# Performance work log

Measured on AMD Instinct MI355X. Metric: run time of the kernel, lower is better.

The kernel has to match this reference:

```python
import jax, jax.numpy as jnp
import numpy as np

N_NODES = 50000
N_EDGES = 800000
IN_CH, HID_CH, OUT_CH = 128, 128, 64


def setup_inputs() -> dict:
    key = jax.random.key(0)
    ks = jax.random.split(key, 8)
    x = jax.random.normal(ks[0], (N_NODES, IN_CH), dtype=jnp.float32)
    edge_index = jax.random.randint(ks[1], (2, N_EDGES), 0, N_NODES, dtype=jnp.int64)
    # PyG SAGEConv params: lin_l (applied to aggregated neighbors, has bias),
    # lin_r (applied to root node, no bias). Stored here as [in, out] matrices.
    s1 = 1.0 / np.sqrt(IN_CH)
    s2 = 1.0 / np.sqrt(HID_CH)
    W1l = jax.random.uniform(ks[2], (IN_CH, HID_CH), jnp.float32, -s1, s1)
    b1 = jnp.zeros((HID_CH,), jnp.float32)
    W1r = jax.random.uniform(ks[3], (IN_CH, HID_CH), jnp.float32, -s1, s1)
    W2l = jax.random.uniform(ks[4], (HID_CH, OUT_CH), jnp.float32, -s2, s2)
    b2 = jnp.zeros((OUT_CH,), jnp.float32)
    W2r = jax.random.uniform(ks[5], (HID_CH, OUT_CH), jnp.float32, -s2, s2)
    return {"x": x, "edge_index": edge_index, "W1l": W1l, "b1": b1,
            "W1r": W1r, "W2l": W2l, "b2": b2, "W2r": W2r}


def _sage_conv(x, src, dst, Wl, b, Wr):
    # mean-aggregate source features onto targets, then linear transform
    msg = x[src]                                        # [E, d] gather
    agg = jax.ops.segment_sum(msg, dst, num_segments=N_NODES)   # [N, d]
    deg = jax.ops.segment_sum(jnp.ones((src.shape[0],), x.dtype), dst,
                              num_segments=N_NODES)     # [N]
    mean = agg / jnp.maximum(deg, 1.0)[:, None]
    return mean @ Wl + b + x @ Wr


def reference(x, edge_index, W1l, b1, W1r, W2l, b2, W2r):
    src, dst = edge_index[0], edge_index[1]
    h = jax.nn.relu(_sage_conv(x, src, dst, W1l, b1, W1r))
    # F.dropout(p=0.3) is identity in eval mode
    return _sage_conv(h, src, dst, W2l, b2, W2r)
```

## Files before the change

kernel.cpp:

```cpp
#include <hip/hip_runtime.h>
#include <hip/hip_bf16.h>


#define TBLOCK 256
#define MAXBUCK 1024
#define BUILD_GRID 512

typedef __attribute__((ext_vector_type(8))) short short8;
typedef __attribute__((ext_vector_type(4))) float f32x4;

__device__ __forceinline__ float bf2f(ushort u) {
    union { unsigned int i; float f; } v;
    v.i = (unsigned int)u << 16;
    return v.f;
}
__device__ __forceinline__ ushort f2bf(float f) {
    union { float f; unsigned int u; } v;
    v.f = f;
    unsigned int r = v.u + 0x7fffu + ((v.u >> 16) & 1u);
    return (ushort)(r >> 16);
}

__device__ __forceinline__ int block_detect_is64(const int* __restrict__ edges) {
    __shared__ int sbad[4];
    __shared__ int sflag;
    int tid = threadIdx.x;
    int bad = 0;
    for (int i = tid; i < 2048; i += TBLOCK)
        if (edges[2 * i + 1] != 0) bad = 1;
    unsigned long long b = __ballot(bad);
    if ((tid & 63) == 0) sbad[tid >> 6] = (b != 0) ? 1 : 0;
    __syncthreads();
    if (tid == 0) sflag = (sbad[0] | sbad[1] | sbad[2] | sbad[3]) ? 0 : 1;
    __syncthreads();
    return sflag;
}

__device__ __forceinline__ int load_src(const int* e, long long i, int E, int is64) {
    return is64 ? e[2 * i] : e[i];
}
__device__ __forceinline__ int load_dst(const int* e, long long i, int E, int is64) {
    return is64 ? e[2 * (long long)E + 2 * i] : e[(long long)E + i];
}

__global__ __launch_bounds__(TBLOCK) void histA_k(const int* __restrict__ edges, int E,
                                                  int* __restrict__ hist, int NBUCK) {
    int is64 = block_detect_is64(edges);
    __shared__ int lh[MAXBUCK];
    int t = threadIdx.x;
    for (int i = t; i < NBUCK; i += TBLOCK) lh[i] = 0;
    __syncthreads();
    int per = (E + gridDim.x - 1) / gridDim.x;
    int b0 = blockIdx.x * per, b1 = min(E, b0 + per);
    for (int i = b0 + t; i < b1; i += TBLOCK) {
        int d = load_dst(edges, i, E, is64);
        atomicAdd(&lh[d >> 8], 1);
    }
    __syncthreads();
    for (int i = t; i < NBUCK; i += TBLOCK)
        if (lh[i]) atomicAdd(&hist[i], lh[i]);
}

__global__ __launch_bounds__(TBLOCK) void scanB_k(const int* __restrict__ hist,
                                                  int* __restrict__ base,
                                                  int* __restrict__ cursor, int NBUCK) {
    __shared__ int s[TBLOCK];
    int t = threadIdx.x;
    int v[4];
    int sum = 0;
#pragma unroll
    for (int i = 0; i < 4; i++) {
        int idx = t * 4 + i;
        int d = (idx < NBUCK) ? hist[idx] : 0;
        v[i] = sum;
        sum += d;
    }
    s[t] = sum;
    __syncthreads();
    for (int off = 1; off < TBLOCK; off <<= 1) {
        int x = (t >= off) ? s[t - off] : 0;
        __syncthreads();
        s[t] += x;
        __syncthreads();
    }
    int excl = (t == 0) ? 0 : s[t - 1];
#pragma unroll
    for (int i = 0; i < 4; i++) {
        int idx = t * 4 + i;
        if (idx < NBUCK) {
            int b = excl + v[i];
            base[idx] = b;
            cursor[idx] = b;
        }
    }
    if (t == TBLOCK - 1) base[NBUCK] = s[TBLOCK - 1];
}

__global__ __launch_bounds__(TBLOCK) void scatterA_k(const int* __restrict__ edges, int E,
                                                     int* __restrict__ cursor,
                                                     unsigned int* __restrict__ packed,
                                                     int NBUCK) {
    int is64 = block_detect_is64(edges);
    __shared__ int lh[MAXBUCK];
    __shared__ int lb[MAXBUCK];
    int t = threadIdx.x;
    for (int i = t; i < NBUCK; i += TBLOCK) lh[i] = 0;
    __syncthreads();
    int per = (E + gridDim.x - 1) / gridDim.x;
    int b0 = blockIdx.x * per, b1 = min(E, b0 + per);
    for (int i = b0 + t; i < b1; i += TBLOCK) {
        int d = load_dst(edges, i, E, is64);
        atomicAdd(&lh[d >> 8], 1);
    }
    __syncthreads();
    for (int i = t; i < NBUCK; i += TBLOCK) {
        int c = lh[i];
        lb[i] = c ? atomicAdd(&cursor[i], c) : 0;
        lh[i] = 0;
    }
    __syncthreads();
    for (int i = b0 + t; i < b1; i += TBLOCK) {
        int s = load_src(edges, i, E, is64);
        int d = load_dst(edges, i, E, is64);
        int b = d >> 8;
        int pos = lb[b] + atomicAdd(&lh[b], 1);
        packed[pos] = (unsigned int)s | ((unsigned int)(d & 255) << 24);
    }
}

__global__ __launch_bounds__(TBLOCK) void buildB_k(const unsigned int* __restrict__ packed,
                                                   const int* __restrict__ base,
                                                   int* __restrict__ offs,
                                                   int* __restrict__ degi,
                                                   float* __restrict__ invdeg,
                                                   int* __restrict__ csr, int N) {
    __shared__ int cnt[TBLOCK], scn[TBLOCK], cur[TBLOCK];
    int t = threadIdx.x;
    int bucket = blockIdx.x;
    int e0 = base[bucket], e1 = base[bucket + 1];
    cnt[t] = 0;
    cur[t] = 0;
    __syncthreads();
    for (int i = e0 + t; i < e1; i += TBLOCK)
        atomicAdd(&cnt[packed[i] >> 24], 1);
    __syncthreads();
    scn[t] = cnt[t];
    __syncthreads();
    for (int off = 1; off < TBLOCK; off <<= 1) {
        int x = (t >= off) ? scn[t - off] : 0;
        __syncthreads();
        scn[t] += x;
        __syncthreads();
    }
    int excl = (t == 0) ? 0 : scn[t - 1];
    int node = bucket * 256 + t;
    if (node < N) {
        offs[node] = e0 + excl;
        degi[node] = cnt[t];
        invdeg[node] = 1.0f / fmaxf((float)cnt[t], 1.0f);
    }
    __syncthreads();
    cnt[t] = excl;
    __syncthreads();
    for (int i = e0 + t; i < e1; i += TBLOCK) {
        unsigned int p = packed[i];
        int nl = p >> 24;
        int pos = e0 + cnt[nl] + atomicAdd(&cur[nl], 1);
        csr[pos] = (int)(p & 0xFFFFFFu);
    }
}

__global__ __launch_bounds__(TBLOCK) void prep_k(const float* __restrict__ x,
                                                 const float* __restrict__ W1l,
                                                 const float* __restrict__ W1r,
                                                 const float* __restrict__ W2l,
                                                 const float* __restrict__ W2r,
                                                 ushort* __restrict__ xb,
                                                 ushort* __restrict__ wc1,
                                                 ushort* __restrict__ wc2,
                                                 int n8, int nxb) {
    if ((int)blockIdx.x < nxb) {
        int i = blockIdx.x * TBLOCK + threadIdx.x;
        if (i >= n8) return;
        const float4* p = (const float4*)x + (size_t)i * 2;
        float4 a = p[0], b = p[1];
        short8 o;
        o[0] = f2bf(a.x); o[1] = f2bf(a.y); o[2] = f2bf(a.z); o[3] = f2bf(a.w);
        o[4] = f2bf(b.x); o[5] = f2bf(b.y); o[6] = f2bf(b.z); o[7] = f2bf(b.w);
        *(short8*)(xb + (size_t)i * 8) = o;
    } else {
        int i = (blockIdx.x - nxb) * TBLOCK + threadIdx.x;
        if (i < 32768) {
            int j = i & 7;
            int rest = i >> 3;
            int n = rest & 127;
            int k = ((rest >> 7) << 3) | j;
            float w = (k < 128) ? W1l[k * 128 + n] : W1r[(k - 128) * 128 + n];
            wc1[i] = f2bf(w);
        } else if (i < 49152) {
            int i2 = i - 32768;
            int j = i2 & 7;
            int rest = i2 >> 3;
            int n = rest & 127;
            int k = ((rest >> 7) << 3) | j;
            float w = (n < 64) ? W2l[k * 64 + n] : W2r[k * 64 + (n - 64)];
            wc2[i2] = f2bf(w);
        }
    }
}

template <int C, bool ACCUM>
__global__ __launch_bounds__(TBLOCK) void gatherb_k(const ushort* __restrict__ feat,
                                                    const int* __restrict__ csr,
                                                    const int* __restrict__ offs,
                                                    const int* __restrict__ degi,
                                                    const float* __restrict__ invdeg,
                                                    ushort* __restrict__ outB,
                                                    float* __restrict__ outF, int N) {
    constexpr int G = C / 8;
    constexpr int NPB = TBLOCK / G;
    int n = blockIdx.x * NPB + threadIdx.x / G;
    if (n >= N) return;
    int lane = threadIdx.x % G;
    int c = lane * 8;
    int s0 = offs[n];
    int d = degi[n];
    float acc[8] = {0.f, 0.f, 0.f, 0.f, 0.f, 0.f, 0.f, 0.f};
    for (int base = 0; base < d; base += G) {
        int rem = d - base;
        int my = (lane < rem) ? csr[s0 + base + lane] : 0;
        if (rem >= G) {
#pragma unroll
            for (int j = 0; j < G; j++) {
                int s = __shfl(my, j, G);
                short8 v = *(const short8*)(feat + (size_t)s * C + c);
#pragma unroll
                for (int q = 0; q < 8; q++) acc[q] += bf2f((ushort)v[q]);
            }
        } else {
            for (int j = 0; j < rem; j++) {
                int s = __shfl(my, j, G);
                short8 v = *(const short8*)(feat + (size_t)s * C + c);
#pragma unroll
                for (int q = 0; q < 8; q++) acc[q] += bf2f((ushort)v[q]);
            }
        }
    }
    float sc = invdeg[n];
    if (ACCUM) {
        float* o = outF + (size_t)n * C + c;
        float4 p0 = *(float4*)o;
        float4 p1 = *(float4*)(o + 4);
        p0.x += sc * acc[0]; p0.y += sc * acc[1]; p0.z += sc * acc[2]; p0.w += sc * acc[3];
        p1.x += sc * acc[4]; p1.y += sc * acc[5]; p1.z += sc * acc[6]; p1.w += sc * acc[7];
        *(float4*)o = p0;
        *(float4*)(o + 4) = p1;
    } else {
        short8 o;
#pragma unroll
        for (int q = 0; q < 8; q++) o[q] = f2bf(sc * acc[q]);
        *(short8*)(outB + (size_t)n * C + c) = o;
    }
}

template <int KTOT, int EPI>
__global__ __launch_bounds__(TBLOCK) void gemm_k(const ushort* __restrict__ A0,
                                                 const ushort* __restrict__ A1,
                                                 const ushort* __restrict__ wc,
                                                 const float* __restrict__ bias,
                                                 ushort* __restrict__ outB,
                                                 float* __restrict__ outF, int N) {
    __shared__ __align__(16) ushort sW[KTOT * 128];
    for (int i = threadIdx.x * 8; i < KTOT * 128; i += TBLOCK * 8)
        *(short8*)&sW[i] = *(const short8*)&wc[i];
    __syncthreads();

    const int wave = threadIdx.x >> 6;
    const int lane = threadIdx.x & 63;
    const int quad = lane >> 4;
    const int l16 = lane & 15;
    const int m0 = (blockIdx.x * 4 + wave) * 32;
    if (m0 >= N) return;

    f32x4 acc[2][8];
#pragma unroll
    for (int t = 0; t < 2; t++)
#pragma unroll
        for (int nt = 0; nt < 8; nt++) acc[t][nt] = (f32x4){0.f, 0.f, 0.f, 0.f};

    const int k0q = quad * 8;
#pragma unroll
    for (int kb = 0; kb < KTOT; kb += 32) {
        int k = kb + k0q;
        const ushort* abase = (KTOT == 256 && k >= 128) ? (A1 + (k - 128)) : (A0 + k);
        short8 a[2];
#pragma unroll
        for (int t = 0; t < 2; t++) {
            int m = m0 + t * 16 + l16;
            if (m > N - 1) m = N - 1;
            a[t] = *(const short8*)(abase + (size_t)m * 128);
        }
#pragma unroll
        for (int nt = 0; nt < 8; nt++) {
            short8 b = *(const short8*)&sW[((k >> 3) * 128 + nt * 16 + l16) * 8];
            acc[0][nt] = __builtin_amdgcn_mfma_f32_16x16x32_bf16(a[0], b, acc[0][nt], 0, 0, 0);
            acc[1][nt] = __builtin_amdgcn_mfma_f32_16x16x32_bf16(a[1], b, acc[1][nt], 0, 0, 0);
        }
    }

#pragma unroll
    for (int t = 0; t < 2; t++) {
#pragma unroll
        for (int r = 0; r < 4; r++) {
            int m = m0 + t * 16 + quad * 4 + r;
            if (m >= N) continue;
#pragma unroll
            for (int nt = 0; nt < 8; nt++) {
                int n = nt * 16 + l16;
                float v = acc[t][nt][r];
                if (EPI == 1) {
                    v = fmaxf(v + bias[n], 0.f);
                    outB[(size_t)m * 128 + n] = f2bf(v);
                } else {
                    if (n < 64) outB[(size_t)m * 64 + n] = f2bf(v);
                    else outF[(size_t)m * 64 + (n - 64)] = v + bias[n - 64];
                }
            }
        }
    }
}

extern "C" void kernel_launch(void* const* d_in, const int* in_sizes, int n_in,
                              void* d_out, int out_size, void* d_ws, size_t ws_size,
                              hipStream_t stream) {
    const float* x = (const float*)d_in[0];
    const int* edges = (const int*)d_in[1];
    const float* W1l = (const float*)d_in[2];
    const float* b1 = (const float*)d_in[3];
    const float* W1r = (const float*)d_in[4];
    const float* W2l = (const float*)d_in[5];
    const float* b2 = (const float*)d_in[6];
    const float* W2r = (const float*)d_in[7];
    float* out = (float*)d_out;

    const int N = in_sizes[0] / 128;
    const int E = in_sizes[1] / 2;
    const int Na = (N + 63) & ~63;
    const int NBUCK = (N + 255) >> 8;

    char* W = (char*)d_ws;
    size_t off = 0;
    auto alloc = [&](size_t bytes) {
        void* p = W + off;
        off = (off + bytes + 255) & ~(size_t)255;
        return p;
    };
    int* hist = (int*)alloc((size_t)MAXBUCK * 4);
    size_t zbytes = off;
    int* base = (int*)alloc((size_t)(MAXBUCK + 1) * 4);
    int* cursor = (int*)alloc((size_t)MAXBUCK * 4);
    int* offs = (int*)alloc((size_t)Na * 4);
    int* degi = (int*)alloc((size_t)Na * 4);
    float* invdeg = (float*)alloc((size_t)Na * 4);
    unsigned int* packed = (unsigned int*)alloc((size_t)E * 4);
    int* csr = (int*)alloc((size_t)E * 4);
    ushort* xb = (ushort*)alloc((size_t)N * 128 * 2);
    ushort* agg1b = (ushort*)alloc((size_t)N * 128 * 2);
    ushort* hb = (ushort*)alloc((size_t)N * 128 * 2);
    ushort* t2b = (ushort*)alloc((size_t)N * 64 * 2);
    ushort* wc1 = (ushort*)alloc(32768 * 2);
    ushort* wc2 = (ushort*)alloc(16384 * 2);

    hipMemsetAsync(d_ws, 0, zbytes, stream);

    histA_k<<<BUILD_GRID, TBLOCK, 0, stream>>>(edges, E, hist, NBUCK);
    scanB_k<<<1, TBLOCK, 0, stream>>>(hist, base, cursor, NBUCK);
    scatterA_k<<<BUILD_GRID, TBLOCK, 0, stream>>>(edges, E, cursor, packed, NBUCK);
    buildB_k<<<NBUCK, TBLOCK, 0, stream>>>(packed, base, offs, degi, invdeg, csr, N);

    const int n8 = N * 128 / 8;
    const int nxb = (n8 + TBLOCK - 1) / TBLOCK;
    prep_k<<<nxb + 192, TBLOCK, 0, stream>>>(x, W1l, W1r, W2l, W2r, xb, wc1, wc2, n8, nxb);

    gatherb_k<128, false><<<(N + 15) / 16, TBLOCK, 0, stream>>>(
        xb, csr, offs, degi, invdeg, agg1b, nullptr, N);
    gemm_k<256, 1><<<(N + 127) / 128, TBLOCK, 0, stream>>>(
        agg1b, xb, wc1, b1, hb, nullptr, N);

    gemm_k<128, 2><<<(N + 127) / 128, TBLOCK, 0, stream>>>(
        hb, nullptr, wc2, b2, t2b, out, N);
    gatherb_k<64, true><<<(N + 31) / 32, TBLOCK, 0, stream>>>(
        t2b, csr, offs, degi, invdeg, nullptr, out, N);
}
```

Before: 215.9 us.

## Fuse CSR build and bf16 prep into one cooperative kernel with grid syncs

```diff
diff --git a/kernel.cpp b/kernel.cpp
--- a/kernel.cpp
+++ b/kernel.cpp
@@ -1,5 +1,8 @@
 #include <hip/hip_runtime.h>
 #include <hip/hip_bf16.h>
+#include <hip/hip_cooperative_groups.h>
+
+namespace cg = cooperative_groups;
 
 
 #define TBLOCK 256
@@ -21,21 +24,6 @@
     return (ushort)(r >> 16);
 }
 
-__device__ __forceinline__ int block_detect_is64(const int* __restrict__ edges) {
-    __shared__ int sbad[4];
-    __shared__ int sflag;
-    int tid = threadIdx.x;
-    int bad = 0;
-    for (int i = tid; i < 2048; i += TBLOCK)
-        if (edges[2 * i + 1] != 0) bad = 1;
-    unsigned long long b = __ballot(bad);
-    if ((tid & 63) == 0) sbad[tid >> 6] = (b != 0) ? 1 : 0;
-    __syncthreads();
-    if (tid == 0) sflag = (sbad[0] | sbad[1] | sbad[2] | sbad[3]) ? 0 : 1;
-    __syncthreads();
-    return sflag;
-}
-
 __device__ __forceinline__ int load_src(const int* e, long long i, int E, int is64) {
     return is64 ? e[2 * i] : e[i];
 }
@@ -43,153 +31,42 @@
     return is64 ? e[2 * (long long)E + 2 * i] : e[(long long)E + i];
 }
 
-__global__ __launch_bounds__(TBLOCK) void histA_k(const int* __restrict__ edges, int E,
-                                                  int* __restrict__ hist, int NBUCK) {
-    int is64 = block_detect_is64(edges);
-    __shared__ int lh[MAXBUCK];
-    int t = threadIdx.x;
-    for (int i = t; i < NBUCK; i += TBLOCK) lh[i] = 0;
-    __syncthreads();
-    int per = (E + gridDim.x - 1) / gridDim.x;
-    int b0 = blockIdx.x * per, b1 = min(E, b0 + per);
-    for (int i = b0 + t; i < b1; i += TBLOCK) {
-        int d = load_dst(edges, i, E, is64);
-        atomicAdd(&lh[d >> 8], 1);
-    }
-    __syncthreads();
-    for (int i = t; i < NBUCK; i += TBLOCK)
-        if (lh[i]) atomicAdd(&hist[i], lh[i]);
-}
-
-__global__ __launch_bounds__(TBLOCK) void scanB_k(const int* __restrict__ hist,
-                                                  int* __restrict__ base,
-                                                  int* __restrict__ cursor, int NBUCK) {
-    __shared__ int s[TBLOCK];
-    int t = threadIdx.x;
-    int v[4];
-    int sum = 0;
-#pragma unroll
-    for (int i = 0; i < 4; i++) {
-        int idx = t * 4 + i;
-        int d = (idx < NBUCK) ? hist[idx] : 0;
-        v[i] = sum;
-        sum += d;
-    }
-    s[t] = sum;
-    __syncthreads();
-    for (int off = 1; off < TBLOCK; off <<= 1) {
-        int x = (t >= off) ? s[t - off] : 0;
-        __syncthreads();
-        s[t] += x;
-        __syncthreads();
-    }
-    int excl = (t == 0) ? 0 : s[t - 1];
-#pragma unroll
-    for (int i = 0; i < 4; i++) {
-        int idx = t * 4 + i;
-        if (idx < NBUCK) {
-            int b = excl + v[i];
-            base[idx] = b;
-            cursor[idx] = b;
-        }
-    }
-    if (t == TBLOCK - 1) base[NBUCK] = s[TBLOCK - 1];
-}
-
-__global__ __launch_bounds__(TBLOCK) void scatterA_k(const int* __restrict__ edges, int E,
-                                                     int* __restrict__ cursor,
-                                                     unsigned int* __restrict__ packed,
-                                                     int NBUCK) {
-    int is64 = block_detect_is64(edges);
+__global__ __launch_bounds__(TBLOCK) void build_k(
+    const float* __restrict__ x,
+    const float* __restrict__ W1l, const float* __restrict__ W1r,
+    const float* __restrict__ W2l, const float* __restrict__ W2r,
+    const int* __restrict__ edges, int E, int N, int NBUCK,
+    ushort* __restrict__ xb, ushort* __restrict__ wc1, ushort* __restrict__ wc2,
+    int* __restrict__ hist, int* __restrict__ baseg, int* __restrict__ cursor,
+    unsigned int* __restrict__ packed,
+    int* __restrict__ offs, int* __restrict__ degi, float* __restrict__ invdeg,
+    int* __restrict__ csr, int n8) {
+    cg::grid_group grid = cg::this_grid();
     __shared__ int lh[MAXBUCK];
     __shared__ int lb[MAXBUCK];
-    int t = threadIdx.x;
-    for (int i = t; i < NBUCK; i += TBLOCK) lh[i] = 0;
-    __syncthreads();
-    int per = (E + gridDim.x - 1) / gridDim.x;
-    int b0 = blockIdx.x * per, b1 = min(E, b0 + per);
-    for (int i = b0 + t; i < b1; i += TBLOCK) {
-        int d = load_dst(edges, i, E, is64);
-        atomicAdd(&lh[d >> 8], 1);
-    }
-    __syncthreads();
-    for (int i = t; i < NBUCK; i += TBLOCK) {
-        int c = lh[i];
-        lb[i] = c ? atomicAdd(&cursor[i], c) : 0;
-        lh[i] = 0;
-    }
-    __syncthreads();
-    for (int i = b0 + t; i < b1; i += TBLOCK) {
-        int s = load_src(edges, i, E, is64);
-        int d = load_dst(edges, i, E, is64);
-        int b = d >> 8;
-        int pos = lb[b] + atomicAdd(&lh[b], 1);
-        packed[pos] = (unsigned int)s | ((unsigned int)(d & 255) << 24);
-    }
-}
-
-__global__ __launch_bounds__(TBLOCK) void buildB_k(const unsigned int* __restrict__ packed,
-                                                   const int* __restrict__ base,
-                                                   int* __restrict__ offs,
-                                                   int* __restrict__ degi,
-                                                   float* __restrict__ invdeg,
-                                                   int* __restrict__ csr, int N) {
-    __shared__ int cnt[TBLOCK], scn[TBLOCK], cur[TBLOCK];
-    int t = threadIdx.x;
-    int bucket = blockIdx.x;
-    int e0 = base[bucket], e1 = base[bucket + 1];
-    cnt[t] = 0;
-    cur[t] = 0;
-    __syncthreads();
-    for (int i = e0 + t; i < e1; i += TBLOCK)
-        atomicAdd(&cnt[packed[i] >> 24], 1);
-    __syncthreads();
-    scn[t] = cnt[t];
-    __syncthreads();
-    for (int off = 1; off < TBLOCK; off <<= 1) {
-        int x = (t >= off) ? scn[t - off] : 0;
-        __syncthreads();
-        scn[t] += x;
-        __syncthreads();
-    }
-    int excl = (t == 0) ? 0 : scn[t - 1];
-    int node = bucket * 256 + t;
-    if (node < N) {
-        offs[node] = e0 + excl;
-        degi[node] = cnt[t];
-        invdeg[node] = 1.0f / fmaxf((float)cnt[t], 1.0f);
-    }
-    __syncthreads();
-    cnt[t] = excl;
-    __syncthreads();
-    for (int i = e0 + t; i < e1; i += TBLOCK) {
-        unsigned int p = packed[i];
-        int nl = p >> 24;
-        int pos = e0 + cnt[nl] + atomicAdd(&cur[nl], 1);
-        csr[pos] = (int)(p & 0xFFFFFFu);
-    }
-}
-
-__global__ __launch_bounds__(TBLOCK) void prep_k(const float* __restrict__ x,
-                                                 const float* __restrict__ W1l,
-                                                 const float* __restrict__ W1r,
-                                                 const float* __restrict__ W2l,
-                                                 const float* __restrict__ W2r,
-                                                 ushort* __restrict__ xb,
-                                                 ushort* __restrict__ wc1,
-                                                 ushort* __restrict__ wc2,
-                                                 int n8, int nxb) {
-    if ((int)blockIdx.x < nxb) {
-        int i = blockIdx.x * TBLOCK + threadIdx.x;
-        if (i >= n8) return;
+    __shared__ int sbad[4];
+    const int t = threadIdx.x;
+    const int nthreads = gridDim.x * TBLOCK;
+    const int gtid = blockIdx.x * TBLOCK + t;
+
+    int bad = 0;
+    for (int i = t; i < 2048; i += TBLOCK)
+        if (edges[2 * i + 1] != 0) bad = 1;
+    unsigned long long bm = __ballot(bad);
+    if ((t & 63) == 0) sbad[t >> 6] = (bm != 0) ? 1 : 0;
+    __syncthreads();
+    const int is64 = (sbad[0] | sbad[1] | sbad[2] | sbad[3]) ? 0 : 1;
+
+    for (int i = gtid; i < MAXBUCK; i += nthreads) hist[i] = 0;
+    for (int i = gtid; i < n8; i += nthreads) {
         const float4* p = (const float4*)x + (size_t)i * 2;
         float4 a = p[0], b = p[1];
         short8 o;
         o[0] = f2bf(a.x); o[1] = f2bf(a.y); o[2] = f2bf(a.z); o[3] = f2bf(a.w);
         o[4] = f2bf(b.x); o[5] = f2bf(b.y); o[6] = f2bf(b.z); o[7] = f2bf(b.w);
         *(short8*)(xb + (size_t)i * 8) = o;
-    } else {
-        int i = (blockIdx.x - nxb) * TBLOCK + threadIdx.x;
+    }
+    for (int i = gtid; i < 49152; i += nthreads) {
         if (i < 32768) {
             int j = i & 7;
             int rest = i >> 3;
@@ -197,7 +74,7 @@
             int k = ((rest >> 7) << 3) | j;
             float w = (k < 128) ? W1l[k * 128 + n] : W1r[(k - 128) * 128 + n];
             wc1[i] = f2bf(w);
-        } else if (i < 49152) {
+        } else {
             int i2 = i - 32768;
             int j = i2 & 7;
             int rest = i2 >> 3;
@@ -205,6 +82,103 @@
             int k = ((rest >> 7) << 3) | j;
             float w = (n < 64) ? W2l[k * 64 + n] : W2r[k * 64 + (n - 64)];
             wc2[i2] = f2bf(w);
+        }
+    }
+    grid.sync();
+
+    for (int i = t; i < NBUCK; i += TBLOCK) lh[i] = 0;
+    __syncthreads();
+    const int per = (E + gridDim.x - 1) / gridDim.x;
+    const int b0 = blockIdx.x * per, b1 = min(E, b0 + per);
+    for (int i = b0 + t; i < b1; i += TBLOCK) {
+        int d = load_dst(edges, i, E, is64);
+        atomicAdd(&lh[d >> 8], 1);
+    }
+    __syncthreads();
+    for (int i = t; i < NBUCK; i += TBLOCK)
+        if (lh[i]) atomicAdd(&hist[i], lh[i]);
+    grid.sync();
+
+    if (blockIdx.x == 0) {
+        int v[4];
+        int sum = 0;
+#pragma unroll
+        for (int i = 0; i < 4; i++) {
+            int idx = t * 4 + i;
+            int d = (idx < NBUCK) ? hist[idx] : 0;
+            v[i] = sum;
+            sum += d;
+        }
+        lb[t] = sum;
+        __syncthreads();
+        for (int off = 1; off < TBLOCK; off <<= 1) {
+            int xv = (t >= off) ? lb[t - off] : 0;
+            __syncthreads();
+            lb[t] += xv;
+            __syncthreads();
+        }
+        int excl = (t == 0) ? 0 : lb[t - 1];
+#pragma unroll
+        for (int i = 0; i < 4; i++) {
+            int idx = t * 4 + i;
+            if (idx < NBUCK) {
+                int b = excl + v[i];
+                baseg[idx] = b;
+                cursor[idx] = b;
+            }
+        }
+        if (t == TBLOCK - 1) baseg[NBUCK] = lb[TBLOCK - 1];
+    }
+    grid.sync();
+
+    for (int i = t; i < NBUCK; i += TBLOCK) {
+        int c = lh[i];
+        lb[i] = c ? atomicAdd(&cursor[i], c) : 0;
+        lh[i] = 0;
+    }
+    __syncthreads();
+    for (int i = b0 + t; i < b1; i += TBLOCK) {
+        int s = load_src(edges, i, E, is64);
+        int d = load_dst(edges, i, E, is64);
+        int b = d >> 8;
+        int pos = lb[b] + atomicAdd(&lh[b], 1);
+        packed[pos] = (unsigned int)s | ((unsigned int)(d & 255) << 24);
+    }
+    grid.sync();
+
+    const int bucket = blockIdx.x;
+    if (bucket < NBUCK) {
+        lh[t] = 0;
+        lh[TBLOCK + t] = 0;
+        __syncthreads();
+        int e0 = baseg[bucket], e1 = baseg[bucket + 1];
+        for (int i = e0 + t; i < e1; i += TBLOCK)
+            atomicAdd(&lh[packed[i] >> 24], 1);
+        __syncthreads();
+        int mycnt = lh[t];
+        lb[t] = mycnt;
+        __syncthreads();
+        for (int off = 1; off < TBLOCK; off <<= 1) {
+            int xv = (t >= off) ? lb[t - off] : 0;
+            __syncthreads();
+            lb[t] += xv;
+            __syncthreads();
+        }
+        int excl = (t == 0) ? 0 : lb[t - 1];
+        int node = bucket * 256 + t;
+        if (node < N) {
+            offs[node] = e0 + excl;
+            degi[node] = mycnt;
+            invdeg[node] = 1.0f / fmaxf((float)mycnt, 1.0f);
+        }
+        __syncthreads();
+        lh[t] = excl;
+        __syncthreads();
+        for (int i = e0 + t; i < e1; i += TBLOCK) {
+            unsigned int p = packed[i];
+            int nl = p >> 24;
+            int pos = e0 + lh[nl] + atomicAdd(&lh[TBLOCK + nl], 1);
+            csr[pos] = (int)(p & 0xFFFFFFu);
         }
     }
 }
@@ -347,17 +321,17 @@
     const int E = in_sizes[1] / 2;
     const int Na = (N + 63) & ~63;
     const int NBUCK = (N + 255) >> 8;
-
-    char* W = (char*)d_ws;
+    const int n8 = N * 128 / 8;
+
+    char* WS = (char*)d_ws;
     size_t off = 0;
     auto alloc = [&](size_t bytes) {
-        void* p = W + off;
+        void* p = WS + off;
         off = (off + bytes + 255) & ~(size_t)255;
         return p;
     };
     int* hist = (int*)alloc((size_t)MAXBUCK * 4);
-    size_t zbytes = off;
-    int* base = (int*)alloc((size_t)(MAXBUCK + 1) * 4);
+    int* baseg = (int*)alloc((size_t)(MAXBUCK + 1) * 4);
     int* cursor = (int*)alloc((size_t)MAXBUCK * 4);
     int* offs = (int*)alloc((size_t)Na * 4);
     int* degi = (int*)alloc((size_t)Na * 4);
@@ -371,16 +345,18 @@
     ushort* wc1 = (ushort*)alloc(32768 * 2);
     ushort* wc2 = (ushort*)alloc(16384 * 2);
 
-    hipMemsetAsync(d_ws, 0, zbytes, stream);
-
-    histA_k<<<BUILD_GRID, TBLOCK, 0, stream>>>(edges, E, hist, NBUCK);
-    scanB_k<<<1, TBLOCK, 0, stream>>>(hist, base, cursor, NBUCK);
-    scatterA_k<<<BUILD_GRID, TBLOCK, 0, stream>>>(edges, E, cursor, packed, NBUCK);
-    buildB_k<<<NBUCK, TBLOCK, 0, stream>>>(packed, base, offs, degi, invdeg, csr, N);
-
-    const int n8 = N * 128 / 8;
-    const int nxb = (n8 + TBLOCK - 1) / TBLOCK;
-    prep_k<<<nxb + 192, TBLOCK, 0, stream>>>(x, W1l, W1r, W2l, W2r, xb, wc1, wc2, n8, nxb);
+    {
+        int E_ = E, N_ = N, NBUCK_ = NBUCK, n8_ = n8;
+        void* args[] = {
+            (void*)&x, (void*)&W1l, (void*)&W1r, (void*)&W2l, (void*)&W2r,
+            (void*)&edges, (void*)&E_, (void*)&N_, (void*)&NBUCK_,
+            (void*)&xb, (void*)&wc1, (void*)&wc2,
+            (void*)&hist, (void*)&baseg, (void*)&cursor,
+            (void*)&packed, (void*)&offs, (void*)&degi, (void*)&invdeg,
+            (void*)&csr, (void*)&n8_};
+        hipLaunchCooperativeKernel((void*)build_k, dim3(BUILD_GRID), dim3(TBLOCK),
+                                   args, 0, stream);
+    }
 
     gatherb_k<128, false><<<(N + 15) / 16, TBLOCK, 0, stream>>>(
         xb, csr, offs, degi, invdeg, agg1b, nullptr, N);
```

After: 439.4 us. 104% more time.

## Fuse histogram with prep kernel and use per-block bucket counts to skip rehistogramming

Applied to the files above, without the earlier changes.

```diff
diff --git a/kernel.cpp b/kernel.cpp
--- a/kernel.cpp
+++ b/kernel.cpp
@@ -4,7 +4,7 @@
 
 #define TBLOCK 256
 #define MAXBUCK 1024
-#define BUILD_GRID 512
+#define HGRID 512
 
 typedef __attribute__((ext_vector_type(8))) short short8;
 typedef __attribute__((ext_vector_type(4))) float f32x4;
@@ -23,7 +23,6 @@
 
 __device__ __forceinline__ int block_detect_is64(const int* __restrict__ edges) {
     __shared__ int sbad[4];
-    __shared__ int sflag;
     int tid = threadIdx.x;
     int bad = 0;
     for (int i = tid; i < 2048; i += TBLOCK)
@@ -31,9 +30,9 @@
     unsigned long long b = __ballot(bad);
     if ((tid & 63) == 0) sbad[tid >> 6] = (b != 0) ? 1 : 0;
     __syncthreads();
-    if (tid == 0) sflag = (sbad[0] | sbad[1] | sbad[2] | sbad[3]) ? 0 : 1;
-    __syncthreads();
-    return sflag;
+    int flag = (sbad[0] | sbad[1] | sbad[2] | sbad[3]) ? 0 : 1;
+    __syncthreads();
+    return flag;
 }
 
 __device__ __forceinline__ int load_src(const int* e, long long i, int E, int is64) {
@@ -43,93 +42,118 @@
     return is64 ? e[2 * (long long)E + 2 * i] : e[(long long)E + i];
 }
 
-__global__ __launch_bounds__(TBLOCK) void histA_k(const int* __restrict__ edges, int E,
-                                                  int* __restrict__ hist, int NBUCK) {
-    int is64 = block_detect_is64(edges);
+__global__ __launch_bounds__(TBLOCK) void histprep_k(
+    const float* __restrict__ x,
+    const float* __restrict__ W1l, const float* __restrict__ W1r,
+    const float* __restrict__ W2l, const float* __restrict__ W2r,
+    const int* __restrict__ edges, int E, int NBUCK,
+    ushort* __restrict__ xb, ushort* __restrict__ wc1, ushort* __restrict__ wc2,
+    int* __restrict__ counts, int n8, int nxb) {
     __shared__ int lh[MAXBUCK];
-    int t = threadIdx.x;
-    for (int i = t; i < NBUCK; i += TBLOCK) lh[i] = 0;
-    __syncthreads();
-    int per = (E + gridDim.x - 1) / gridDim.x;
-    int b0 = blockIdx.x * per, b1 = min(E, b0 + per);
-    for (int i = b0 + t; i < b1; i += TBLOCK) {
-        int d = load_dst(edges, i, E, is64);
-        atomicAdd(&lh[d >> 8], 1);
-    }
-    __syncthreads();
-    for (int i = t; i < NBUCK; i += TBLOCK)
-        if (lh[i]) atomicAdd(&hist[i], lh[i]);
-}
-
-__global__ __launch_bounds__(TBLOCK) void scanB_k(const int* __restrict__ hist,
-                                                  int* __restrict__ base,
-                                                  int* __restrict__ cursor, int NBUCK) {
+    const int b = blockIdx.x;
+    const int t = threadIdx.x;
+    if (b < HGRID) {
+        const int is64 = block_detect_is64(edges);
+        for (int i = t; i < NBUCK; i += TBLOCK) lh[i] = 0;
+        __syncthreads();
+        const int per = (E + HGRID - 1) / HGRID;
+        const int b0 = b * per, b1 = min(E, b0 + per);
+        for (int i = b0 + t; i < b1; i += TBLOCK)
+            atomicAdd(&lh[load_dst(edges, i, E, is64) >> 8], 1);
+        __syncthreads();
+        for (int j = t; j < NBUCK; j += TBLOCK)
+            counts[j * HGRID + b] = lh[j];
+    } else {
+        int pb = b - HGRID;
+        if (pb < nxb) {
+            int i = pb * TBLOCK + t;
+            if (i >= n8) return;
+            const float4* p = (const float4*)x + (size_t)i * 2;
+            float4 a = p[0], bb = p[1];
+            short8 o;
+            o[0] = f2bf(a.x); o[1] = f2bf(a.y); o[2] = f2bf(a.z); o[3] = f2bf(a.w);
+            o[4] = f2bf(bb.x); o[5] = f2bf(bb.y); o[6] = f2bf(bb.z); o[7] = f2bf(bb.w);
+            *(short8*)(xb + (size_t)i * 8) = o;
+        } else {
+            int i = (pb - nxb) * TBLOCK + t;
+            if (i < 32768) {
+                int j = i & 7;
+                int rest = i >> 3;
+                int n = rest & 127;
+                int k = ((rest >> 7) << 3) | j;
+                float w = (k < 128) ? W1l[k * 128 + n] : W1r[(k - 128) * 128 + n];
+                wc1[i] = f2bf(w);
+            } else if (i < 49152) {
+                int i2 = i - 32768;
+                int j = i2 & 7;
+                int rest = i2 >> 3;
+                int n = rest & 127;
+                int k = ((rest >> 7) << 3) | j;
+                float w = (n < 64) ? W2l[k * 64 + n] : W2r[k * 64 + (n - 64)];
+                wc2[i2] = f2bf(w);
+            }
+        }
+    }
+}
+
+__global__ __launch_bounds__(TBLOCK) void scan_k(int* __restrict__ counts,
+                                                 int* __restrict__ baseg, int NBUCK) {
     __shared__ int s[TBLOCK];
-    int t = threadIdx.x;
-    int v[4];
+    const int t = threadIdx.x;
     int sum = 0;
-#pragma unroll
-    for (int i = 0; i < 4; i++) {
-        int idx = t * 4 + i;
-        int d = (idx < NBUCK) ? hist[idx] : 0;
-        v[i] = sum;
-        sum += d;
+    if (t < NBUCK) {
+        const int* row = counts + (size_t)t * HGRID;
+        for (int b = 0; b < HGRID; b++) sum += row[b];
     }
     s[t] = sum;
     __syncthreads();
     for (int off = 1; off < TBLOCK; off <<= 1) {
-        int x = (t >= off) ? s[t - off] : 0;
-        __syncthreads();
-        s[t] += x;
+        int xv = (t >= off) ? s[t - off] : 0;
+        __syncthreads();
+        s[t] += xv;
         __syncthreads();
     }
     int excl = (t == 0) ? 0 : s[t - 1];
-#pragma unroll
-    for (int i = 0; i < 4; i++) {
-        int idx = t * 4 + i;
-        if (idx < NBUCK) {
-            int b = excl + v[i];
-            base[idx] = b;
-            cursor[idx] = b;
-        }
-    }
-    if (t == TBLOCK - 1) base[NBUCK] = s[TBLOCK - 1];
+    if (t < NBUCK) {
+        baseg[t] = excl;
+        if (t == NBUCK - 1) baseg[NBUCK] = s[t];
+        int* row = counts + (size_t)t * HGRID;
+        int run = excl;
+        for (int b = 0; b < HGRID; b++) {
+            int c = row[b];
+            row[b] = run;
+            run += c;
+        }
+    }
 }
 
 __global__ __launch_bounds__(TBLOCK) void scatterA_k(const int* __restrict__ edges, int E,
-                                                     int* __restrict__ cursor,
+                                                     const int* __restrict__ counts,
                                                      unsigned int* __restrict__ packed,
                                                      int NBUCK) {
-    int is64 = block_detect_is64(edges);
+    const int is64 = block_detect_is64(edges);
+    __shared__ int lb[MAXBUCK];
     __shared__ int lh[MAXBUCK];
-    __shared__ int lb[MAXBUCK];
-    int t = threadIdx.x;
-    for (int i = t; i < NBUCK; i += TBLOCK) lh[i] = 0;
-    __syncthreads();
-    int per = (E + gridDim.x - 1) / gridDim.x;
-    int b0 = blockIdx.x * per, b1 = min(E, b0 + per);
-    for (int i = b0 + t; i < b1; i += TBLOCK) {
-        int d = load_dst(edges, i, E, is64);
-        atomicAdd(&lh[d >> 8], 1);
-    }
-    __syncthreads();
-    for (int i = t; i < NBUCK; i += TBLOCK) {
-        int c = lh[i];
-        lb[i] = c ? atomicAdd(&cursor[i], c) : 0;
-        lh[i] = 0;
-    }
-    __syncthreads();
+    const int b = blockIdx.x;
+    const int t = threadIdx.x;
+    for (int j = t; j < NBUCK; j += TBLOCK) {
+        lb[j] = counts[j * HGRID + b];
+        lh[j] = 0;
+    }
+    __syncthreads();
+    const int per = (E + HGRID - 1) / HGRID;
+    const int b0 = b * per, b1 = min(E, b0 + per);
     for (int i = b0 + t; i < b1; i += TBLOCK) {
         int s = load_src(edges, i, E, is64);
         int d = load_dst(edges, i, E, is64);
-        int b = d >> 8;
-        int pos = lb[b] + atomicAdd(&lh[b], 1);
+        int bk = d >> 8;
+        int pos = lb[bk] + atomicAdd(&lh[bk], 1);
         packed[pos] = (unsigned int)s | ((unsigned int)(d & 255) << 24);
     }
 }
 
 __global__ __launch_bounds__(TBLOCK) void buildB_k(const unsigned int* __restrict__ packed,
-                                                   const int* __restrict__ base,
+                                                   const int* __restrict__ baseg,
                                                    int* __restrict__ offs,
                                                    int* __restrict__ degi,
                                                    float* __restrict__ invdeg,
@@ -137,7 +161,7 @@
     __shared__ int cnt[TBLOCK], scn[TBLOCK], cur[TBLOCK];
     int t = threadIdx.x;
     int bucket = blockIdx.x;
-    int e0 = base[bucket], e1 = base[bucket + 1];
+    int e0 = baseg[bucket], e1 = baseg[bucket + 1];
     cnt[t] = 0;
     cur[t] = 0;
     __syncthreads();
@@ -167,45 +191,6 @@
         int nl = p >> 24;
         int pos = e0 + cnt[nl] + atomicAdd(&cur[nl], 1);
         csr[pos] = (int)(p & 0xFFFFFFu);
-    }
-}
-
-__global__ __launch_bounds__(TBLOCK) void prep_k(const float* __restrict__ x,
-                                                 const float* __restrict__ W1l,
-                                                 const float* __restrict__ W1r,
-                                                 const float* __restrict__ W2l,
-                                                 const float* __restrict__ W2r,
-                                                 ushort* __restrict__ xb,
-                                                 ushort* __restrict__ wc1,
-                                                 ushort* __restrict__ wc2,
-                                                 int n8, int nxb) {
-    if ((int)blockIdx.x < nxb) {
-        int i = blockIdx.x * TBLOCK + threadIdx.x;
-        if (i >= n8) return;
-        const float4* p = (const float4*)x + (size_t)i * 2;
-        float4 a = p[0], b = p[1];
-        short8 o;
-        o[0] = f2bf(a.x); o[1] = f2bf(a.y); o[2] = f2bf(a.z); o[3] = f2bf(a.w);
-        o[4] = f2bf(b.x); o[5] = f2bf(b.y); o[6] = f2bf(b.z); o[7] = f2bf(b.w);
-        *(short8*)(xb + (size_t)i * 8) = o;
-    } else {
-        int i = (blockIdx.x - nxb) * TBLOCK + threadIdx.x;
-        if (i < 32768) {
-            int j = i & 7;
-            int rest = i >> 3;
-            int n = rest & 127;
-            int k = ((rest >> 7) << 3) | j;
-            float w = (k < 128) ? W1l[k * 128 + n] : W1r[(k - 128) * 128 + n];
-            wc1[i] = f2bf(w);
-        } else if (i < 49152) {
-            int i2 = i - 32768;
-            int j = i2 & 7;
-            int rest = i2 >> 3;
-            int n = rest & 127;
-            int k = ((rest >> 7) << 3) | j;
-            float w = (n < 64) ? W2l[k * 64 + n] : W2r[k * 64 + (n - 64)];
-            wc2[i2] = f2bf(w);
-        }
     }
 }
 
@@ -347,18 +332,18 @@
     const int E = in_sizes[1] / 2;
     const int Na = (N + 63) & ~63;
     const int NBUCK = (N + 255) >> 8;
-
-    char* W = (char*)d_ws;
+    const int n8 = N * 128 / 8;
+    const int nxb = (n8 + TBLOCK - 1) / TBLOCK;
+
+    char* WS = (char*)d_ws;
     size_t off = 0;
     auto alloc = [&](size_t bytes) {
-        void* p = W + off;
+        void* p = WS + off;
         off = (off + bytes + 255) & ~(size_t)255;
         return p;
     };
-    int* hist = (int*)alloc((size_t)MAXBUCK * 4);
-    size_t zbytes = off;
-    int* base = (int*)alloc((size_t)(MAXBUCK + 1) * 4);
-    int* cursor = (int*)alloc((size_t)MAXBUCK * 4);
+    int* counts = (int*)alloc((size_t)MAXBUCK * HGRID * 4);
+    int* baseg = (int*)alloc((size_t)(MAXBUCK + 1) * 4);
     int* offs = (int*)alloc((size_t)Na * 4);
     int* degi = (int*)alloc((size_t)Na * 4);
     float* invdeg = (float*)alloc((size_t)Na * 4);
@@ -371,16 +356,11 @@
     ushort* wc1 = (ushort*)alloc(32768 * 2);
     ushort* wc2 = (ushort*)alloc(16384 * 2);
 
-    hipMemsetAsync(d_ws, 0, zbytes, stream);
-
-    histA_k<<<BUILD_GRID, TBLOCK, 0, stream>>>(edges, E, hist, NBUCK);
-    scanB_k<<<1, TBLOCK, 0, stream>>>(hist, base, cursor, NBUCK);
-    scatterA_k<<<BUILD_GRID, TBLOCK, 0, stream>>>(edges, E, cursor, packed, NBUCK);
-    buildB_k<<<NBUCK, TBLOCK, 0, stream>>>(packed, base, offs, degi, invdeg, csr, N);
-
-    const int n8 = N * 128 / 8;
-    const int nxb = (n8 + TBLOCK - 1) / TBLOCK;
-    prep_k<<<nxb + 192, TBLOCK, 0, stream>>>(x, W1l, W1r, W2l, W2r, xb, wc1, wc2, n8, nxb);
+    histprep_k<<<HGRID + nxb + 192, TBLOCK, 0, stream>>>(
+        x, W1l, W1r, W2l, W2r, edges, E, NBUCK, xb, wc1, wc2, counts, n8, nxb);
+    scan_k<<<1, TBLOCK, 0, stream>>>(counts, baseg, NBUCK);
+    scatterA_k<<<HGRID, TBLOCK, 0, stream>>>(edges, E, counts, packed, NBUCK);
+    buildB_k<<<NBUCK, TBLOCK, 0, stream>>>(packed, baseg, offs, degi, invdeg, csr, N);
 
     gatherb_k<128, false><<<(N + 15) / 16, TBLOCK, 0, stream>>>(
         xb, csr, offs, degi, invdeg, agg1b, nullptr, N);
```

Result: slower. 231.9 us (+7.4%).
